# Kernel optimization log

Hardware: AMD Instinct MI355X
Metric: run time of the kernel (lower is better)

The kernel has to match this reference:

```python
import jax, jax.numpy as jnp
import numpy as np

ALPHA = 1.0

def setup_inputs() -> dict:
    key = jax.random.key(0)
    kx, kd = jax.random.split(key)
    B, L, D = 64, 256, 512
    x = jax.random.normal(kx, (B, L, D), dtype=jnp.float32)
    duration = jax.random.randint(kd, (B, L), 0, 8, dtype=jnp.int32)
    max_length = 1792  # L * max_duration
    return {"x": x, "duration": duration, "max_length": max_length}

def reference(x, duration, max_length):
    B, L, D = x.shape
    # round(duration * alpha) -> integer durations
    d = jnp.round(duration.astype(jnp.float32) * ALPHA).astype(jnp.int32)
    # rows with all-zero durations get one frame (original picks a random
    # position; we deterministically use position 0)
    row_sum = d.sum(axis=1)  # [B]
    d = jnp.where((row_sum == 0)[:, None] & (jnp.arange(L) == 0)[None, :], 1, d)
    # cumulative end offsets per phoneme: cum[b, j] = sum_{k<=j} d[b, k]
    cum = jnp.cumsum(d, axis=1)  # [B, L]
    t = jnp.arange(max_length)   # [T]
    # output frame t belongs to phoneme j where cum[j-1] <= t < cum[j]
    idx = jax.vmap(lambda c: jnp.searchsorted(c, t, side='right'))(cum)  # [B, T]
    idx = jnp.clip(idx, 0, L - 1)
    out = jnp.take_along_axis(x, idx[:, :, None], axis=1)  # [B, T, D]
    # zero-pad beyond each sequence's total length
    mask = (t[None, :] < cum[:, -1:]).astype(x.dtype)  # [B, T]
    out = out * mask[:, :, None]
    return out, max_length
```

## Files before the change

kernel.cpp:

```cpp
#include <hip/hip_runtime.h>


#define BB 64
#define LL 256
#define DD 512
#define TT 1792
#define D4 (DD / 4)

__global__ __launch_bounds__(256) void length_regulator_kernel(
    const float4* __restrict__ x4,
    const int*    __restrict__ dur,
    const int*    __restrict__ maxlen,
    float*        __restrict__ out)
{
    __shared__ int cum[LL];
    const int tid = threadIdx.x;
    const int b   = blockIdx.y;

    cum[tid] = dur[b * LL + tid];
    __syncthreads();
    #pragma unroll
    for (int off = 1; off < LL; off <<= 1) {
        int v = (tid >= off) ? cum[tid - off] : 0;
        __syncthreads();
        cum[tid] += v;
        __syncthreads();
    }
    int total = cum[LL - 1];
    if (total == 0) cum[tid] = 1;
    __syncthreads();
    total = cum[LL - 1];

    float4* out4 = (float4*)out;
    const int group  = tid >> 7;
    const int lane   = tid & 127;
    const int t_base = blockIdx.x * 16;

    #pragma unroll
    for (int j = 0; j < 8; ++j) {
        const int t = t_base + j * 2 + group;
        float4 val = make_float4(0.f, 0.f, 0.f, 0.f);
        if (t < total) {
            int lo = 0, hi = LL;
            while (lo < hi) {
                const int mid = (lo + hi) >> 1;
                if (cum[mid] <= t) lo = mid + 1; else hi = mid;
            }
            const int idx = (lo < LL - 1) ? lo : (LL - 1);
            val = x4[((size_t)b * LL + idx) * D4 + lane];
        }
        out4[((size_t)b * TT + t) * D4 + lane] = val;
    }

    if (b == 0 && blockIdx.x == 0 && tid == 0) {
        out[(size_t)BB * TT * DD] = (float)maxlen[0];
    }
}

extern "C" void kernel_launch(void* const* d_in, const int* in_sizes, int n_in,
                              void* d_out, int out_size, void* d_ws, size_t ws_size,
                              hipStream_t stream) {
    const float4* x4  = (const float4*)d_in[0];
    const int*    dur = (const int*)d_in[1];
    const int*    ml  = (const int*)d_in[2];
    float*        out = (float*)d_out;

    dim3 grid(TT / 16, BB);
    length_regulator_kernel<<<grid, dim3(256), 0, stream>>>(x4, dur, ml, out);
}
```

Baseline: 270.4 us.

## Replace per-frame binary search with shared-memory scatter index table and streaming stores

Each block now scatters phoneme indices into a shared table covering its tile of output frames, instead of running a binary search for every frame. The tile size doubles so the per-block prefix-sum cost is spread over more frames. Output stores use nontemporal hints to avoid polluting the cache. This adds an extra sync and serial scatter loops per thread, and halves the grid size.

```diff
diff --git a/kernel.cpp b/kernel.cpp
--- a/kernel.cpp
+++ b/kernel.cpp
@@ -6,16 +6,21 @@
 #define DD 512
 #define TT 1792
 #define D4 (DD / 4)
+#define TILE 32
+
+typedef float vfloat4 __attribute__((ext_vector_type(4)));
 
 __global__ __launch_bounds__(256) void length_regulator_kernel(
-    const float4* __restrict__ x4,
-    const int*    __restrict__ dur,
-    const int*    __restrict__ maxlen,
-    float*        __restrict__ out)
+    const vfloat4* __restrict__ x4,
+    const int*     __restrict__ dur,
+    const int*     __restrict__ maxlen,
+    float*         __restrict__ out)
 {
     __shared__ int cum[LL];
+    __shared__ int sidx[TILE];
     const int tid = threadIdx.x;
     const int b   = blockIdx.y;
+    const int t0  = blockIdx.x * TILE;
 
     cum[tid] = dur[b * LL + tid];
     __syncthreads();
@@ -31,25 +36,29 @@
     __syncthreads();
     total = cum[LL - 1];
 
-    float4* out4 = (float4*)out;
-    const int group  = tid >> 7;
-    const int lane   = tid & 127;
-    const int t_base = blockIdx.x * 16;
+    if (tid < TILE) sidx[tid] = 0;
+    __syncthreads();
+    {
+        const int end   = cum[tid];
+        const int start = (tid == 0) ? 0 : cum[tid - 1];
+        const int s = max(start, t0);
+        const int e = min(end, t0 + TILE);
+        for (int t = s; t < e; ++t) sidx[t - t0] = tid;
+    }
+    __syncthreads();
+
+    vfloat4* out4 = (vfloat4*)out;
+    const int group = tid >> 7;
+    const int lane  = tid & 127;
 
     #pragma unroll
-    for (int j = 0; j < 8; ++j) {
-        const int t = t_base + j * 2 + group;
-        float4 val = make_float4(0.f, 0.f, 0.f, 0.f);
+    for (int j = 0; j < TILE / 2; ++j) {
+        const int t = t0 + j * 2 + group;
+        vfloat4 val = (vfloat4)(0.f);
         if (t < total) {
-            int lo = 0, hi = LL;
-            while (lo < hi) {
-                const int mid = (lo + hi) >> 1;
-                if (cum[mid] <= t) lo = mid + 1; else hi = mid;
-            }
-            const int idx = (lo < LL - 1) ? lo : (LL - 1);
-            val = x4[((size_t)b * LL + idx) * D4 + lane];
+            val = x4[((size_t)b * LL + sidx[t - t0]) * D4 + lane];
         }
-        out4[((size_t)b * TT + t) * D4 + lane] = val;
+        __builtin_nontemporal_store(val, &out4[((size_t)b * TT + t) * D4 + lane]);
     }
 
     if (b == 0 && blockIdx.x == 0 && tid == 0) {
@@ -60,11 +69,11 @@
 extern "C" void kernel_launch(void* const* d_in, const int* in_sizes, int n_in,
                               void* d_out, int out_size, void* d_ws, size_t ws_size,
                               hipStream_t stream) {
-    const float4* x4  = (const float4*)d_in[0];
-    const int*    dur = (const int*)d_in[1];
-    const int*    ml  = (const int*)d_in[2];
-    float*        out = (float*)d_out;
+    const vfloat4* x4  = (const vfloat4*)d_in[0];
+    const int*     dur = (const int*)d_in[1];
+    const int*     ml  = (const int*)d_in[2];
+    float*         out = (float*)d_out;
 
-    dim3 grid(TT / 16, BB);
+    dim3 grid(TT / TILE, BB);
     length_regulator_kernel<<<grid, dim3(256), 0, stream>>>(x4, dur, ml, out);
 }
```

New measurement: 271.6 us. Within noise of the previous version (+0.4%).
